# Kernel optimization log

Measured on AMD Instinct MI355X. Metric: run time of the kernel, lower is better.

Reference implementation:

```python
import jax, jax.numpy as jnp
import numpy as np
from jax import lax

B, R, C_FEAT, HF, WF = 4, 512, 256, 50, 50
NUM_CLASSES = 91
POOL = 7
SCALE = 1.0 / 16.0
IMG_H = IMG_W = 800.0
SCORE_THRESH = 0.05
NMS_THRESH = 0.5
DETS_PER_IMG = 100
TOPK_NMS = 2048  # fixed-size candidate set for static-shape NMS
BBOX_W = np.array([10.0, 10.0, 5.0, 5.0], np.float32)
BBOX_CLIP = float(np.log(1000.0 / 16.0))
MIN_SIZE = 0.01


def setup_inputs():
    key = jax.random.key(0)
    ks = jax.random.split(key, 8)
    features = jax.random.normal(ks[0], (B, C_FEAT, HF, WF), jnp.float32)
    cxy = jax.random.uniform(ks[1], (B, R, 2), jnp.float32, 50.0, 750.0)
    wh = jax.random.uniform(ks[2], (B, R, 2), jnp.float32, 20.0, 200.0)
    proposals = jnp.concatenate([cxy - wh / 2, cxy + wh / 2], axis=-1)
    d_in = C_FEAT * POOL * POOL
    def lin(k, fi, fo):
        return jax.random.normal(k, (fi, fo), jnp.float32) / np.sqrt(fi)
    return {
        'features': features, 'proposals': proposals,
        'W1': lin(ks[3], d_in, 1024), 'b1': jnp.zeros((1024,), jnp.float32),
        'W2': lin(ks[4], 1024, 1024), 'b2': jnp.zeros((1024,), jnp.float32),
        'Wc': lin(ks[5], 1024, NUM_CLASSES), 'bc': jnp.zeros((NUM_CLASSES,), jnp.float32),
        'Wr': lin(ks[6], 1024, 4 * NUM_CLASSES), 'br': jnp.zeros((4 * NUM_CLASSES,), jnp.float32),
    }


def roi_align(features, proposals):
    # features [B,C,H,W], proposals [B,R,4] in image coords -> [B*R, C*POOL*POOL]
    featT = jnp.transpose(features, (0, 2, 3, 1))  # [B,H,W,C]
    boxes = proposals * SCALE
    x1, y1, x2, y2 = (boxes[..., i] for i in range(4))
    bh = (y2 - y1) / POOL
    bw = (x2 - x1) / POOL
    centers = jnp.arange(POOL, dtype=jnp.float32) + 0.5
    ys = y1[..., None] + centers * bh[..., None]  # [B,R,P]
    xs = x1[..., None] + centers * bw[..., None]  # [B,R,P]

    def bil(fT, ys_b, xs_b):  # per-image bilinear sampling
        yy = jnp.broadcast_to(ys_b[:, :, None], (R, POOL, POOL))
        xx = jnp.broadcast_to(xs_b[:, None, :], (R, POOL, POOL))
        y = jnp.clip(yy, 0.0, HF - 1.0)
        x = jnp.clip(xx, 0.0, WF - 1.0)
        y0 = jnp.floor(y); x0 = jnp.floor(x)
        y0i = y0.astype(jnp.int32); x0i = x0.astype(jnp.int32)
        y1i = jnp.minimum(y0i + 1, HF - 1); x1i = jnp.minimum(x0i + 1, WF - 1)
        ly = y - y0; lx = x - x0; hy = 1.0 - ly; hx = 1.0 - lx
        f00 = fT[y0i, x0i]; f01 = fT[y0i, x1i]
        f10 = fT[y1i, x0i]; f11 = fT[y1i, x1i]  # [R,P,P,C]
        out = ((hy * hx)[..., None] * f00 + (hy * lx)[..., None] * f01 +
               (ly * hx)[..., None] * f10 + (ly * lx)[..., None] * f11)
        return out  # [R,P,P,C]

    pooled = jax.vmap(bil)(featT, ys, xs)  # [B,R,P,P,C]
    pooled = jnp.transpose(pooled, (0, 1, 4, 2, 3))  # [B,R,C,P,P] (torch layout)
    return pooled.reshape(B * R, -1)


def decode_boxes(box_reg, props):
    # box_reg [N, 4*NC], props [N,4] -> [N,NC,4]
    w = props[:, 2] - props[:, 0]
    h = props[:, 3] - props[:, 1]
    cx = props[:, 0] + 0.5 * w
    cy = props[:, 1] + 0.5 * h
    d = box_reg.reshape(-1, NUM_CLASSES, 4) / jnp.asarray(BBOX_W)
    dx, dy = d[..., 0], d[..., 1]
    dw = jnp.minimum(d[..., 2], BBOX_CLIP)
    dh = jnp.minimum(d[..., 3], BBOX_CLIP)
    pcx = dx * w[:, None] + cx[:, None]
    pcy = dy * h[:, None] + cy[:, None]
    pw = jnp.exp(dw) * w[:, None]
    ph = jnp.exp(dh) * h[:, None]
    return jnp.stack([pcx - 0.5 * pw, pcy - 0.5 * ph,
                      pcx + 0.5 * pw, pcy + 0.5 * ph], axis=-1)


def box_iou(a, b):
    area_a = (a[:, 2] - a[:, 0]) * (a[:, 3] - a[:, 1])
    area_b = (b[:, 2] - b[:, 0]) * (b[:, 3] - b[:, 1])
    lt = jnp.maximum(a[:, None, :2], b[None, :, :2])
    rb = jnp.minimum(a[:, None, 2:], b[None, :, 2:])
    wh = jnp.clip(rb - lt, 0.0)
    inter = wh[..., 0] * wh[..., 1]
    return inter / (area_a[:, None] + area_b[None, :] - inter)


def post_image(boxes, scores):
    # boxes [R,NC,4], scores [R,NC] -> fixed-size top DETS_PER_IMG detections
    x1 = jnp.clip(boxes[..., 0], 0.0, IMG_W)
    y1 = jnp.clip(boxes[..., 1], 0.0, IMG_H)
    x2 = jnp.clip(boxes[..., 2], 0.0, IMG_W)
    y2 = jnp.clip(boxes[..., 3], 0.0, IMG_H)
    boxes = jnp.stack([x1, y1, x2, y2], axis=-1)
    # drop background class 0, flatten (roi, class) candidates
    boxes = boxes[:, 1:].reshape(-1, 4)            # [R*(NC-1),4]
    scores = scores[:, 1:].reshape(-1)
    labels = jnp.broadcast_to(jnp.arange(1, NUM_CLASSES, dtype=jnp.int32)[None, :],
                              (R, NUM_CLASSES - 1)).reshape(-1)
    wv = boxes[:, 2] - boxes[:, 0]
    hv = boxes[:, 3] - boxes[:, 1]
    valid = (scores > SCORE_THRESH) & (wv >= MIN_SIZE) & (hv >= MIN_SIZE)
    cand = jnp.where(valid, scores, -1.0)
    top_s, top_i = lax.top_k(cand, TOPK_NMS)       # sorted desc by score
    b_k = boxes[top_i]
    l_k = labels[top_i]
    v_k = valid[top_i]
    # batched (per-class) NMS via label offset
    off = l_k.astype(jnp.float32)[:, None] * (IMG_W + 1.0)
    iou = box_iou(b_k + off, b_k + off)            # [K,K]
    idx = jnp.arange(TOPK_NMS)

    def body(i, keep):
        sup = jnp.any((idx < i) & keep & (iou[:, i] > NMS_THRESH))
        return keep.at[i].set(keep[i] & ~sup)

    keep = lax.fori_loop(0, TOPK_NMS, body, v_k)
    fs = jnp.where(keep, top_s, -1.0)
    out_s, out_i = lax.top_k(fs, DETS_PER_IMG)
    ok = out_s > 0.0
    out_b = jnp.where(ok[:, None], b_k[out_i], 0.0)
    out_l = jnp.where(ok, l_k[out_i], 0)
    out_s = jnp.where(ok, out_s, 0.0)
    return out_b, out_s, out_l


def reference(features, proposals, W1, b1, W2, b2, Wc, bc, Wr, br):
    x = roi_align(features, proposals)               # [B*R, C*49]
    x = jax.nn.relu(x @ W1 + b1)
    x = jax.nn.relu(x @ W2 + b2)
    class_logits = x @ Wc + bc                        # [B*R, NC]
    box_regression = x @ Wr + br                      # [B*R, 4*NC]
    props_flat = proposals.reshape(-1, 4)
    pred_boxes = decode_boxes(box_regression, props_flat).reshape(B, R, NUM_CLASSES, 4)
    pred_scores = jax.nn.softmax(class_logits, axis=-1).reshape(B, R, NUM_CLASSES)
    boxes, scores, labels = jax.vmap(post_image)(pred_boxes, pred_scores)
    return boxes, scores, labels


if __name__ == '__main__':
    out = reference(**setup_inputs())
    print([o.shape for o in out])
```

## Files before the change

kernel.cpp:

```cpp
#include <hip/hip_runtime.h>
#include <stdint.h>

#define NBI 4
#define RRI 512
#define NROI 2048
#define DIN 12544
#define BBOX_CLIP_F 4.135166556742356f

typedef _Float16 half8 __attribute__((ext_vector_type(8)));
typedef float f32x16 __attribute__((ext_vector_type(16)));

#define O_AH      10240000ull
#define O_AL      61620224ull
#define O_WTH     113000448ull
#define O_WTL     138690560ull
#define OZ        164380672ull
#define WS_NEED   189546496ull

#define O_X2H     0ull
#define O_X2L     2097152ull
#define O_X1H     O_AH
#define O_X1L     (O_AH + 4194304ull)
#define O_PBOX    O_AL
#define O_KEYS    (O_AL + 2949120ull)
#define O_NMSBOX  (O_AL + 3473408ull)
#define O_OUTBOX  (O_AL + 3604480ull)
#define O_SCORE   (O_AL + 3735552ull)
#define O_LABEL   (O_AL + 3768320ull)
#define O_CNT     (O_AL + 3801088ull)
#define O_MASK    (O_AL + 3802112ull)
#define O_WHH     O_WTH
#define O_WHL     (O_WTH + 1048576ull)
#define O_BH      (O_WTH + 2097152ull)
#define O_PARTH   (O_WTH + 2101248ull)
#define O_HEADF   (O_WTH + 18878464ull)
#define O_W2TH    OZ
#define O_W2TL    (OZ + 2097152ull)
#define O_PFC2    (OZ + 4194304ull)

__global__ void k_zero_out(float* __restrict__ out) {
  int i = blockIdx.x * 256 + threadIdx.x;
  if (i < 2400) out[i] = 0.0f;
}

__global__ void k_zero2(unsigned* __restrict__ keys32, unsigned* __restrict__ cnt) {
  int i = blockIdx.x * 256 + threadIdx.x;
  if (i < 131072) keys32[i] = 0u;
  if (i < 64) cnt[i] = 0u;
}

__global__ __launch_bounds__(256) void k_transpose(const float* __restrict__ f,
                                                   float* __restrict__ ft) {
  __shared__ float s[32][33];
  int b = blockIdx.z;
  int hw0 = blockIdx.x << 5;
  int c0 = blockIdx.y << 5;
  int tx = threadIdx.x & 31, ty = threadIdx.x >> 5;
#pragma unroll
  for (int j = 0; j < 32; j += 8) {
    int hw = hw0 + tx;
    if (hw < 2500) s[ty + j][tx] = f[((size_t)b * 256 + c0 + ty + j) * 2500 + hw];
  }
  __syncthreads();
#pragma unroll
  for (int j = 0; j < 32; j += 8) {
    int hw = hw0 + ty + j;
    if (hw < 2500) ft[((size_t)b * 2500 + hw) * 256 + c0 + tx] = s[tx][ty + j];
  }
}

__global__ __launch_bounds__(256) void k_wsplit(const float* __restrict__ W,
                                                _Float16* __restrict__ Th,
                                                _Float16* __restrict__ Tl, int K, int N) {
  __shared__ float s[64][68];
  int k0 = blockIdx.x << 6, n0 = blockIdx.y << 6;
  int t = threadIdx.x;
  int r = t >> 2, c4 = (t & 3) << 4;
#pragma unroll
  for (int j = 0; j < 16; j += 4) {
    float4 v = *(const float4*)(W + (size_t)(k0 + r) * N + n0 + c4 + j);
    s[r][c4 + j] = v.x; s[r][c4 + j + 1] = v.y; s[r][c4 + j + 2] = v.z; s[r][c4 + j + 3] = v.w;
  }
  __syncthreads();
  int nr = t >> 2, kc = (t & 3) << 4;
  half8 h8[2], l8[2];
#pragma unroll
  for (int j = 0; j < 16; ++j) {
    float v = s[kc + j][nr];
    _Float16 h = (_Float16)v;
    _Float16 lo = (_Float16)((v - (float)h) * 2048.0f);
    h8[j >> 3][j & 7] = h;
    l8[j >> 3][j & 7] = lo;
  }
  size_t base = (size_t)(n0 + nr) * K + k0 + kc;
  *(half8*)(Th + base) = h8[0]; *(half8*)(Th + base + 8) = h8[1];
  *(half8*)(Tl + base) = l8[0]; *(half8*)(Tl + base + 8) = l8[1];
}

__global__ __launch_bounds__(256) void k_wsplit_heads(const float* __restrict__ Wc,
                                                      const float* __restrict__ Wr,
                                                      const float* __restrict__ bcv,
                                                      const float* __restrict__ brv,
                                                      _Float16* __restrict__ Th,
                                                      _Float16* __restrict__ Tl,
                                                      float* __restrict__ bh) {
  int n = blockIdx.x;
  int t = threadIdx.x;
  for (int k = t; k < 1024; k += 256) {
    float v = (n < 91) ? Wc[(size_t)k * 91 + n]
                       : ((n < 455) ? Wr[(size_t)k * 364 + (n - 91)] : 0.0f);
    _Float16 h = (_Float16)v;
    Th[(size_t)n * 1024 + k] = h;
    Tl[(size_t)n * 1024 + k] = (_Float16)((v - (float)h) * 2048.0f);
  }
  if (t == 0) bh[n] = (n < 91) ? bcv[n] : ((n < 455) ? brv[n - 91] : 0.0f);
}

__global__ __launch_bounds__(256) void k_roialign(const float* __restrict__ ft,
                                                  const float* __restrict__ props,
                                                  _Float16* __restrict__ Ahg,
                                                  _Float16* __restrict__ Alg) {
  __shared__ float pool[DIN];
  __shared__ float lyA[7], lxA[7];
  __shared__ int y0A[7], y1A[7], x0A[7], x1A[7];
  int roi = blockIdx.x;
  int b = roi >> 9;
  const float* p = props + (size_t)roi * 4;
  float x1s = p[0] * 0.0625f, y1s = p[1] * 0.0625f;
  float x2s = p[2] * 0.0625f, y2s = p[3] * 0.0625f;
  float bh = (y2s - y1s) / 7.0f;
  float bw = (x2s - x1s) / 7.0f;
  int t = threadIdx.x;
  if (t < 7) {
    float y = y1s + ((float)t + 0.5f) * bh;
    y = fminf(fmaxf(y, 0.0f), 49.0f);
    float y0 = floorf(y);
    int y0i = (int)y0;
    y0A[t] = y0i; y1A[t] = min(y0i + 1, 49); lyA[t] = y - y0;
  } else if (t < 14) {
    int px = t - 7;
    float x = x1s + ((float)px + 0.5f) * bw;
    x = fminf(fmaxf(x, 0.0f), 49.0f);
    float x0 = floorf(x);
    int x0i = (int)x0;
    x0A[px] = x0i; x1A[px] = min(x0i + 1, 49); lxA[px] = x - x0;
  }
  __syncthreads();
  const float* fb = ft + (size_t)b * 2500 * 256;
  int c = t;
  for (int p49 = 0; p49 < 49; ++p49) {
    int py = p49 / 7, px = p49 - py * 7;
    int y0 = y0A[py], y1 = y1A[py], x0 = x0A[px], x1 = x1A[px];
    float ly = lyA[py], lx = lxA[px], hy = 1.0f - ly, hx = 1.0f - lx;
    float f00 = fb[(y0 * 50 + x0) * 256 + c];
    float f01 = fb[(y0 * 50 + x1) * 256 + c];
    float f10 = fb[(y1 * 50 + x0) * 256 + c];
    float f11 = fb[(y1 * 50 + x1) * 256 + c];
    pool[c * 49 + p49] = (hy * hx) * f00 + (hy * lx) * f01 + (ly * hx) * f10 + (ly * lx) * f11;
  }
  __syncthreads();
  _Float16* dh = Ahg + (size_t)roi * DIN;
  _Float16* dl = Alg + (size_t)roi * DIN;
  for (int i = t; i < DIN; i += 256) {
    float v = pool[i];
    _Float16 h = (_Float16)v;
    dh[i] = h;
    dl[i] = (_Float16)((v - (float)h) * 2048.0f);
  }
}

__global__ __launch_bounds__(256, 2) void k_mfma(const _Float16* __restrict__ Ah,
                                                 const _Float16* __restrict__ Al,
                                                 const _Float16* __restrict__ Bh,
                                                 const _Float16* __restrict__ Bl,
                                                 float* __restrict__ P0,
                                                 float* __restrict__ P2,
                                                 int K, int K2, int ldc, int MN) {
  __shared__ __align__(16) half8 sA[2][2][512];
  __shared__ __align__(16) half8 sB[2][2][512];
  int gx = gridDim.x, gy = gridDim.y;
  int nwg = gx * gy * gridDim.z;
  int lin = blockIdx.x + gx * (blockIdx.y + gy * blockIdx.z);
  int cpx = nwg >> 3;
  int nl = (lin & 7) * cpx + (lin >> 3);
  int sx = __ffs(gx) - 1, sy = __ffs(gy) - 1;
  int lx = nl & (gx - 1);
  int rest = nl >> sx;
  int ly = rest & (gy - 1);
  int lz = rest >> sy;
  int m0 = ly << 7, n0 = lx << 7;
  int kb = lz * K2;
  int t = threadIdx.x;
  int w = t >> 6, l = t & 63;
  int wr = w >> 1, wc = w & 1;
  int fr = l & 31, cgrp = l >> 5;
  int sr = t >> 1, sh = t & 1;
  const _Float16* gAh = Ah + (size_t)(m0 + sr) * K + kb + sh * 16;
  const _Float16* gAl = Al + (size_t)(m0 + sr) * K + kb + sh * 16;
  const _Float16* gBh = Bh + (size_t)(n0 + sr) * K + kb + sh * 16;
  const _Float16* gBl = Bl + (size_t)(n0 + sr) * K + kb + sh * 16;
  int ws0 = ((sr >> 5) * 4 + 2 * sh) * 32 + (sr & 31);
  int ws1 = ws0 + 32;
  int sa0 = wr * 256 + cgrp * 32 + fr;
  int sb0 = wc * 256 + cgrp * 32 + fr;
  f32x16 accH[2][2], accL[2][2];
#pragma unroll
  for (int i = 0; i < 2; ++i)
#pragma unroll
    for (int j = 0; j < 2; ++j)
#pragma unroll
      for (int r = 0; r < 16; ++r) { accH[i][j][r] = 0.0f; accL[i][j][r] = 0.0f; }
  half8 rAh0 = *(const half8*)gAh, rAh1 = *(const half8*)(gAh + 8);
  half8 rAl0 = *(const half8*)gAl, rAl1 = *(const half8*)(gAl + 8);
  half8 rBh0 = *(const half8*)gBh, rBh1 = *(const half8*)(gBh + 8);
  half8 rBl0 = *(const half8*)gBl, rBl1 = *(const half8*)(gBl + 8);
  sA[0][0][ws0] = rAh0; sA[0][0][ws1] = rAh1;
  sA[0][1][ws0] = rAl0; sA[0][1][ws1] = rAl1;
  sB[0][0][ws0] = rBh0; sB[0][0][ws1] = rBh1;
  sB[0][1][ws0] = rBl0; sB[0][1][ws1] = rBl1;
  if (32 < K2) {
    rAh0 = *(const half8*)(gAh + 32); rAh1 = *(const half8*)(gAh + 40);
    rAl0 = *(const half8*)(gAl + 32); rAl1 = *(const half8*)(gAl + 40);
    rBh0 = *(const half8*)(gBh + 32); rBh1 = *(const half8*)(gBh + 40);
    rBl0 = *(const half8*)(gBl + 32); rBl1 = *(const half8*)(gBl + 40);
  }
  __syncthreads();
  for (int kt = 0; kt < K2; kt += 32) {
    int buf = (kt >> 5) & 1;
    bool more = (kt + 32) < K2;
    if (more) {
      sA[buf ^ 1][0][ws0] = rAh0; sA[buf ^ 1][0][ws1] = rAh1;
      sA[buf ^ 1][1][ws0] = rAl0; sA[buf ^ 1][1][ws1] = rAl1;
      sB[buf ^ 1][0][ws0] = rBh0; sB[buf ^ 1][0][ws1] = rBh1;
      sB[buf ^ 1][1][ws0] = rBl0; sB[buf ^ 1][1][ws1] = rBl1;
    }
    if ((kt + 64) < K2) {
      rAh0 = *(const half8*)(gAh + kt + 64); rAh1 = *(const half8*)(gAh + kt + 72);
      rAl0 = *(const half8*)(gAl + kt + 64); rAl1 = *(const half8*)(gAl + kt + 72);
      rBh0 = *(const half8*)(gBh + kt + 64); rBh1 = *(const half8*)(gBh + kt + 72);
      rBl0 = *(const half8*)(gBl + kt + 64); rBl1 = *(const half8*)(gBl + kt + 72);
    }
#pragma unroll
    for (int s = 0; s < 2; ++s) {
      half8 aH[2], aL[2], bH[2], bL[2];
#pragma unroll
      for (int mf = 0; mf < 2; ++mf) {
        int sa = sa0 + mf * 128 + s * 64;
        aH[mf] = sA[buf][0][sa];
        aL[mf] = sA[buf][1][sa];
      }
#pragma unroll
      for (int nf = 0; nf < 2; ++nf) {
        int sb = sb0 + nf * 128 + s * 64;
        bH[nf] = sB[buf][0][sb];
        bL[nf] = sB[buf][1][sb];
      }
#pragma unroll
      for (int mf = 0; mf < 2; ++mf)
#pragma unroll
        for (int nf = 0; nf < 2; ++nf) {
          accH[mf][nf] =
              __builtin_amdgcn_mfma_f32_32x32x16_f16(aH[mf], bH[nf], accH[mf][nf], 0, 0, 0);
          accL[mf][nf] =
              __builtin_amdgcn_mfma_f32_32x32x16_f16(aH[mf], bL[nf], accL[mf][nf], 0, 0, 0);
          accL[mf][nf] =
              __builtin_amdgcn_mfma_f32_32x32x16_f16(aL[mf], bH[nf], accL[mf][nf], 0, 0, 0);
        }
    }
    if (more) __syncthreads();
  }
  float* Pz = (lz == 2) ? P2 : (P0 + (size_t)(lz == 3 ? 2 : lz) * MN);
  const float sc = 4.8828125e-4f;
#pragma unroll
  for (int mf = 0; mf < 2; ++mf)
#pragma unroll
    for (int nf = 0; nf < 2; ++nf) {
      int col = n0 + wc * 64 + nf * 32 + fr;
      int rbase = m0 + wr * 64 + mf * 32 + 4 * cgrp;
#pragma unroll
      for (int r = 0; r < 16; ++r) {
        int row = rbase + (r & 3) + ((r >> 2) << 3);
        Pz[(size_t)row * ldc + col] = accH[mf][nf][r] + accL[mf][nf][r] * sc;
      }
    }
}

__global__ void k_reduce_split(const float* __restrict__ P0, const float* __restrict__ P2,
                               const float* __restrict__ bias, _Float16* __restrict__ xh,
                               _Float16* __restrict__ xl, int S) {
  const int MN = 2048 * 1024;
  int i8 = blockIdx.x * 256 + threadIdx.x;
  size_t base = (size_t)i8 * 8;
  float v[8];
  {
    float4 a0 = *(const float4*)(P0 + base);
    float4 a1 = *(const float4*)(P0 + base + 4);
    float4 b0 = *(const float4*)(P0 + MN + base);
    float4 b1 = *(const float4*)(P0 + MN + base + 4);
    v[0] = a0.x + b0.x; v[1] = a0.y + b0.y; v[2] = a0.z + b0.z; v[3] = a0.w + b0.w;
    v[4] = a1.x + b1.x; v[5] = a1.y + b1.y; v[6] = a1.z + b1.z; v[7] = a1.w + b1.w;
  }
  if (S == 4) {
    float4 c0 = *(const float4*)(P2 + base);
    float4 c1 = *(const float4*)(P2 + base + 4);
    float4 d0 = *(const float4*)(P0 + 2 * (size_t)MN + base);
    float4 d1 = *(const float4*)(P0 + 2 * (size_t)MN + base + 4);
    v[0] = (v[0] + c0.x) + d0.x; v[1] = (v[1] + c0.y) + d0.y;
    v[2] = (v[2] + c0.z) + d0.z; v[3] = (v[3] + c0.w) + d0.w;
    v[4] = (v[4] + c1.x) + d1.x; v[5] = (v[5] + c1.y) + d1.y;
    v[6] = (v[6] + c1.z) + d1.z; v[7] = (v[7] + c1.w) + d1.w;
  }
  int cb = (int)(base & 1023);
  float4 b0 = *(const float4*)(bias + cb);
  float4 b1v = *(const float4*)(bias + cb + 4);
  v[0] += b0.x; v[1] += b0.y; v[2] += b0.z; v[3] += b0.w;
  v[4] += b1v.x; v[5] += b1v.y; v[6] += b1v.z; v[7] += b1v.w;
  half8 h8, l8;
#pragma unroll
  for (int j = 0; j < 8; ++j) {
    float x = fmaxf(v[j], 0.0f);
    _Float16 h = (_Float16)x;
    h8[j] = h;
    l8[j] = (_Float16)((x - (float)h) * 2048.0f);
  }
  *(half8*)(xh + base) = h8;
  *(half8*)(xl + base) = l8;
}

__global__ void k_headreduce(const float4* __restrict__ PH, const float* __restrict__ bh,
                             float4* __restrict__ head) {
  const int MN4 = 2048 * 512 / 4;
  int i = blockIdx.x * 256 + threadIdx.x;
  float4 p0 = PH[i], p1 = PH[i + MN4], p2 = PH[i + 3 * MN4], p3 = PH[i + 2 * MN4];
  const float4 b = *(const float4*)(bh + ((i & 127) << 2));
  float4 o;
  o.x = ((p0.x + p1.x) + p2.x) + p3.x + b.x;
  o.y = ((p0.y + p1.y) + p2.y) + p3.y + b.y;
  o.z = ((p0.z + p1.z) + p2.z) + p3.z + b.z;
  o.w = ((p0.w + p1.w) + p2.w) + p3.w + b.w;
  head[i] = o;
}

__global__ __launch_bounds__(256) void k_softmax_decode(const float* __restrict__ head,
                                                        const float* __restrict__ props,
                                                        float* __restrict__ pbox,
                                                        unsigned long long* __restrict__ keys,
                                                        unsigned* __restrict__ cnt) {
  int wave = threadIdx.x >> 6, lane = threadIdx.x & 63;
  int roi = (blockIdx.x << 2) + wave;
  const float* hr = head + (size_t)roi * 512;
  float l0 = hr[lane];
  float l1 = (lane < 27) ? hr[lane + 64] : -3.4e38f;
  float m = fmaxf(l0, l1);
#pragma unroll
  for (int off = 32; off; off >>= 1) m = fmaxf(m, __shfl_xor(m, off));
  float e0 = expf(l0 - m);
  float e1 = (lane < 27) ? expf(l1 - m) : 0.0f;
  float ssum = e0 + e1;
#pragma unroll
  for (int off = 32; off; off >>= 1) ssum += __shfl_xor(ssum, off);
  const float* pr = props + (size_t)roi * 4;
  float w = pr[2] - pr[0], h = pr[3] - pr[1];
  float cx = pr[0] + 0.5f * w, cy = pr[1] + 0.5f * h;
  int img = roi >> 9, rl = roi & 511;
#pragma unroll
  for (int half = 0; half < 2; ++half) {
    int c = lane + half * 64;
    float e = half ? e1 : e0;
    if (c >= 1 && c <= 90) {
      float score = e / ssum;
      const float* rg = hr + 91 + (c << 2);
      float dx = rg[0] / 10.0f, dy = rg[1] / 10.0f;
      float dw = fminf(rg[2] / 5.0f, BBOX_CLIP_F);
      float dh = fminf(rg[3] / 5.0f, BBOX_CLIP_F);
      float pcx = dx * w + cx, pcy = dy * h + cy;
      float pw = expf(dw) * w, ph = expf(dh) * h;
      float bx1 = pcx - 0.5f * pw, by1 = pcy - 0.5f * ph;
      float bx2 = pcx + 0.5f * pw, by2 = pcy + 0.5f * ph;
      bx1 = fminf(fmaxf(bx1, 0.0f), 800.0f);
      by1 = fminf(fmaxf(by1, 0.0f), 800.0f);
      bx2 = fminf(fmaxf(bx2, 0.0f), 800.0f);
      by2 = fminf(fmaxf(by2, 0.0f), 800.0f);
      float* pb = pbox + ((size_t)roi * 90 + (c - 1)) * 4;
      pb[0] = bx1; pb[1] = by1; pb[2] = bx2; pb[3] = by2;
      if (score > 0.05f && (bx2 - bx1) >= 0.01f && (by2 - by1) >= 0.01f) {
        unsigned pos = atomicAdd(cnt + img, 1u);
        unsigned idx = (unsigned)rl * 90u + (unsigned)(c - 1);
        unsigned su = __float_as_uint(score);
        su ^= (su >> 31) ? 0xFFFFFFFFu : 0x80000000u;
        keys[((size_t)img << 14) + pos] =
            ((unsigned long long)su << 32) | (unsigned long long)(0xFFFFFFFFu - idx);
      }
    }
  }
}

__global__ void k_sort(unsigned long long* __restrict__ keys, const unsigned* __restrict__ cnt) {
  extern __shared__ unsigned long long s[];
  int img = blockIdx.x, tid = threadIdx.x;
  unsigned long long* kb = keys + ((size_t)img << 14);
  unsigned n = cnt[img];
  unsigned np = 2048; while (np < n && np < 16384) np <<= 1;
  if (np <= 8192) {
    for (unsigned i = tid; i < np; i += 1024) s[i] = kb[i];
    __syncthreads();
    for (unsigned k = 2; k <= np; k <<= 1) {
      for (unsigned j = k >> 1; j; j >>= 1) {
        for (unsigned x = tid; x < (np >> 1); x += 1024) {
          unsigned i = ((x & ~(j - 1)) << 1) | (x & (j - 1));
          unsigned l = i | j;
          bool up = ((i & k) == 0);
          unsigned long long a = s[i], b = s[l];
          if ((a > b) == up) { s[i] = b; s[l] = a; }
        }
        __syncthreads();
      }
    }
    for (unsigned i = tid; i < np; i += 1024) kb[i] = s[i];
  } else {
    for (int ch = 0; ch < 2; ++ch) {
      unsigned base = (unsigned)ch << 13;
      for (unsigned i = tid; i < 8192; i += 1024) s[i] = kb[base + i];
      __syncthreads();
      for (unsigned k = 2; k <= 8192; k <<= 1) {
        for (unsigned j = k >> 1; j; j >>= 1) {
          for (unsigned x = tid; x < 4096; x += 1024) {
            unsigned i = ((x & ~(j - 1)) << 1) | (x & (j - 1));
            unsigned l = i | j;
            bool up = (((base + i) & k) == 0);
            unsigned long long a = s[i], b = s[l];
            if ((a > b) == up) { s[i] = b; s[l] = a; }
          }
          __syncthreads();
        }
      }
      for (unsigned i = tid; i < 8192; i += 1024) kb[base + i] = s[i];
      __syncthreads();
    }
    for (unsigned x = tid; x < 8192; x += 1024) {
      unsigned long long a = kb[x], b = kb[x + 8192];
      if (a > b) { kb[x] = b; kb[x + 8192] = a; }
    }
    __syncthreads();
    for (int ch = 0; ch < 2; ++ch) {
      unsigned base = (unsigned)ch << 13;
      for (unsigned i = tid; i < 8192; i += 1024) s[i] = kb[base + i];
      __syncthreads();
      for (unsigned j = 4096; j; j >>= 1) {
        for (unsigned x = tid; x < 4096; x += 1024) {
          unsigned i = ((x & ~(j - 1)) << 1) | (x & (j - 1));
          unsigned l = i | j;
          unsigned long long a = s[i], b = s[l];
          if (a > b) { s[i] = b; s[l] = a; }
        }
        __syncthreads();
      }
      for (unsigned i = tid; i < 8192; i += 1024) kb[base + i] = s[i];
      __syncthreads();
    }
  }
}

__global__ void k_gather(const unsigned long long* __restrict__ keys,
                         const unsigned* __restrict__ cnt, const float* __restrict__ pbox,
                         float4* __restrict__ nmsbox, float4* __restrict__ outbox,
                         float* __restrict__ score, float* __restrict__ label) {
  int g = blockIdx.x * 256 + threadIdx.x;
  int img = g >> 11, slot = g & 2047;
  unsigned n = cnt[img];
  unsigned neff = n > 2048u ? 2048u : n;
  unsigned np = 2048; while (np < n && np < 16384) np <<= 1;
  float4 bo = make_float4(0, 0, 0, 0), bx = make_float4(0, 0, 0, 0);
  float sc = -1.0f, lb = 0.0f;
  if ((unsigned)slot < neff) {
    unsigned long long key = keys[((size_t)img << 14) + (np - 1 - slot)];
    unsigned su = (unsigned)(key >> 32);
    su = (su & 0x80000000u) ? (su ^ 0x80000000u) : ~su;
    sc = __uint_as_float(su);
    unsigned idx = 0xFFFFFFFFu - (unsigned)(key & 0xFFFFFFFFull);
    unsigned rl = idx / 90u, c = idx - rl * 90u;
    const float* pb = pbox + ((size_t)((img << 9) + rl) * 90 + c) * 4;
    bx = *(const float4*)pb;
    float off = (float)(c + 1) * 801.0f;
    bo = make_float4(bx.x + off, bx.y + off, bx.z + off, bx.w + off);
    lb = (float)(c + 1);
  }
  nmsbox[g] = bo; outbox[g] = bx; score[g] = sc; label[g] = lb;
}

__global__ __launch_bounds__(256) void k_mask(const float* __restrict__ nmsbox,
                                              unsigned* __restrict__ mask) {
  __shared__ float bx[2048 * 4];
  int img = blockIdx.x >> 9;
  int i0 = (blockIdx.x & 511) << 2;
  const float4* src = (const float4*)(nmsbox + (size_t)img * 2048 * 4);
  for (int q = threadIdx.x; q < 2048; q += 256) ((float4*)bx)[q] = src[q];
  __syncthreads();
  int w = threadIdx.x & 63, ir = threadIdx.x >> 6;
  int i = i0 + ir;
  float ax1 = bx[i * 4], ay1 = bx[i * 4 + 1], ax2 = bx[i * 4 + 2], ay2 = bx[i * 4 + 3];
  float areaA = (ax2 - ax1) * (ay2 - ay1);
  unsigned bits = 0;
  for (int jj = 0; jj < 32; ++jj) {
    int j2 = (jj + w) & 31;
    int j = (w << 5) + j2;
    float b1 = bx[j * 4], b2 = bx[j * 4 + 1], b3 = bx[j * 4 + 2], b4 = bx[j * 4 + 3];
    float areaB = (b3 - b1) * (b4 - b2);
    float lx = fmaxf(ax1, b1), lyv = fmaxf(ay1, b2);
    float rx = fminf(ax2, b3), ry = fminf(ay2, b4);
    float iw = fmaxf(rx - lx, 0.0f), ih = fmaxf(ry - lyv, 0.0f);
    float inter = iw * ih;
    float iou = inter / (areaA + areaB - inter);
    if (iou > 0.5f) bits |= (1u << j2);
  }
  mask[((size_t)img * 2048 + i) * 64 + w] = bits;
}

__global__ void k_scan(const unsigned* __restrict__ mask, const unsigned* __restrict__ cnt,
                       const float* __restrict__ outbox, const float* __restrict__ score,
                       const float* __restrict__ label, float* __restrict__ dout) {
  int img = blockIdx.x, lane = threadIdx.x;
  unsigned n = cnt[img];
  unsigned neff = n > 2048u ? 2048u : n;
  unsigned base = (unsigned)lane * 32u;
  unsigned rem;
  if (base + 32u <= neff) rem = 0u;
  else if (base >= neff) rem = 0xFFFFFFFFu;
  else rem = ~((1u << (neff - base)) - 1u);
  const unsigned* mrow = mask + (size_t)img * 2048 * 64;
  unsigned row = (neff > 0) ? mrow[lane] : 0u;
  int outc = 0;
  for (int i = 0; i < (int)neff; ++i) {
    unsigned nextrow = (i + 1 < (int)neff) ? mrow[(size_t)(i + 1) * 64 + lane] : 0u;
    unsigned wrd = __shfl(rem, i >> 5);
    bool kept = ((wrd >> (i & 31)) & 1u) == 0u;
    if (kept) {
      rem |= row;
      if (lane < 4)
        dout[(size_t)(img * 100 + outc) * 4 + lane] = outbox[((size_t)img * 2048 + i) * 4 + lane];
      if (lane == 0) {
        dout[1600 + img * 100 + outc] = score[img * 2048 + i];
        dout[2000 + img * 100 + outc] = label[img * 2048 + i];
      }
      ++outc;
      if (outc >= 100) break;
    }
    row = nextrow;
  }
}

extern "C" void kernel_launch(void* const* d_in, const int* in_sizes, int n_in,
                              void* d_out, int out_size, void* d_ws, size_t ws_size,
                              hipStream_t stream) {
  if (ws_size < WS_NEED) return;

  const float* features  = (const float*)d_in[0];
  const float* proposals = (const float*)d_in[1];
  const float* W1 = (const float*)d_in[2];
  const float* b1 = (const float*)d_in[3];
  const float* W2 = (const float*)d_in[4];
  const float* b2 = (const float*)d_in[5];
  const float* Wc = (const float*)d_in[6];
  const float* bc = (const float*)d_in[7];
  const float* Wr = (const float*)d_in[8];
  const float* br = (const float*)d_in[9];
  float* out = (float*)d_out;
  char* ws = (char*)d_ws;

  float* featT = (float*)(ws + 0);
  _Float16* Ahg = (_Float16*)(ws + O_AH);
  _Float16* Alg = (_Float16*)(ws + O_AL);
  _Float16* Wth = (_Float16*)(ws + O_WTH);
  _Float16* Wtl = (_Float16*)(ws + O_WTL);
  float* partZ = (float*)(ws + OZ);
  float* partF = (float*)(ws + 0);
  _Float16* x1h = (_Float16*)(ws + O_X1H);
  _Float16* x1l = (_Float16*)(ws + O_X1L);
  _Float16* W2th = (_Float16*)(ws + O_W2TH);
  _Float16* W2tl = (_Float16*)(ws + O_W2TL);
  float* partC = (float*)(ws + O_PFC2);
  _Float16* x2h = (_Float16*)(ws + O_X2H);
  _Float16* x2l = (_Float16*)(ws + O_X2L);
  _Float16* whh = (_Float16*)(ws + O_WHH);
  _Float16* whl = (_Float16*)(ws + O_WHL);
  float* bhv   = (float*)(ws + O_BH);
  float* partH = (float*)(ws + O_PARTH);
  float* partH2 = (float*)(ws + O_PARTH + 3ull * 4194304ull);
  float* head  = (float*)(ws + O_HEADF);
  float* pbox  = (float*)(ws + O_PBOX);
  unsigned long long* keys = (unsigned long long*)(ws + O_KEYS);
  float* nmsbox = (float*)(ws + O_NMSBOX);
  float* outbox = (float*)(ws + O_OUTBOX);
  float* scorea = (float*)(ws + O_SCORE);
  float* labela = (float*)(ws + O_LABEL);
  unsigned* cnt = (unsigned*)(ws + O_CNT);
  unsigned* maska = (unsigned*)(ws + O_MASK);

  k_zero_out<<<10, 256, 0, stream>>>(out);
  k_transpose<<<dim3(79, 8, 4), 256, 0, stream>>>(features, featT);
  k_wsplit<<<dim3(196, 16), 256, 0, stream>>>(W1, Wth, Wtl, 12544, 1024);
  k_roialign<<<2048, 256, 0, stream>>>(featT, proposals, Ahg, Alg);
  k_mfma<<<dim3(8, 16, 4), 256, 0, stream>>>(Ahg, Alg, Wth, Wtl, partZ, partF,
                                             12544, 3136, 1024, 2048 * 1024);
  k_reduce_split<<<1024, 256, 0, stream>>>(partZ, partF, b1, x1h, x1l, 4);
  k_wsplit<<<dim3(16, 16), 256, 0, stream>>>(W2, W2th, W2tl, 1024, 1024);
  k_wsplit_heads<<<512, 256, 0, stream>>>(Wc, Wr, bc, br, whh, whl, bhv);
  k_mfma<<<dim3(8, 16, 2), 256, 0, stream>>>(x1h, x1l, W2th, W2tl, partC, partC,
                                             1024, 512, 1024, 2048 * 1024);
  k_reduce_split<<<1024, 256, 0, stream>>>(partC, partC, b2, x2h, x2l, 2);
  k_mfma<<<dim3(4, 16, 4), 256, 0, stream>>>(x2h, x2l, whh, whl, partH, partH2,
                                             1024, 256, 512, 2048 * 512);
  k_headreduce<<<1024, 256, 0, stream>>>((const float4*)partH, bhv, (float4*)head);
  k_zero2<<<512, 256, 0, stream>>>((unsigned*)keys, cnt);
  k_softmax_decode<<<512, 256, 0, stream>>>(head, proposals, pbox, keys, cnt);
  k_sort<<<4, 1024, 65536, stream>>>(keys, cnt);
  k_gather<<<32, 256, 0, stream>>>(keys, cnt, pbox, (float4*)nmsbox, (float4*)outbox,
                                   scorea, labela);
  k_mask<<<2048, 256, 0, stream>>>(nmsbox, maska);
  k_scan<<<4, 64, 0, stream>>>(maska, cnt, outbox, scorea, labela, out);
}
```

Baseline: 383.8 us.

## Use direct global-to-LDS loads in MFMA GEMM and fuse small prep kernels

The MFMA GEMM now stages A and B tiles with `global_load_lds` straight into shared memory, replacing the register round-trip and its separate LDS stores. Several tiny launches are folded into neighbours: output zeroing moves into the transpose, W2 split plus head-weight split plus key zeroing become one kernel, and the head partial reduction is done inside softmax/decode. The RoI-align output conversion writes 8-wide half vectors instead of scalars. These aim to cut launch overhead, an extra global round-trip for the head logits, and GEMM load latency. The catch is that direct-to-LDS loads depend on correct wait and barrier ordering, and softmax now re-reads four partials per element.

```diff
diff --git a/kernel.cpp b/kernel.cpp
--- a/kernel.cpp
+++ b/kernel.cpp
@@ -9,6 +9,10 @@
 
 typedef _Float16 half8 __attribute__((ext_vector_type(8)));
 typedef float f32x16 __attribute__((ext_vector_type(16)));
+
+#define GLDS(g, l)                                                                   \
+  __builtin_amdgcn_global_load_lds((const __attribute__((address_space(1))) void*)(g), \
+                                   (__attribute__((address_space(3))) void*)(l), 16, 0, 0)
 
 #define O_AH      10240000ull
 #define O_AL      61620224ull
@@ -33,28 +37,21 @@
 #define O_WHL     (O_WTH + 1048576ull)
 #define O_BH      (O_WTH + 2097152ull)
 #define O_PARTH   (O_WTH + 2101248ull)
-#define O_HEADF   (O_WTH + 18878464ull)
 #define O_W2TH    OZ
 #define O_W2TL    (OZ + 2097152ull)
 #define O_PFC2    (OZ + 4194304ull)
 
-__global__ void k_zero_out(float* __restrict__ out) {
-  int i = blockIdx.x * 256 + threadIdx.x;
-  if (i < 2400) out[i] = 0.0f;
-}
-
-__global__ void k_zero2(unsigned* __restrict__ keys32, unsigned* __restrict__ cnt) {
-  int i = blockIdx.x * 256 + threadIdx.x;
-  if (i < 131072) keys32[i] = 0u;
-  if (i < 64) cnt[i] = 0u;
-}
-
 __global__ __launch_bounds__(256) void k_transpose(const float* __restrict__ f,
-                                                   float* __restrict__ ft) {
+                                                   float* __restrict__ ft,
+                                                   float* __restrict__ out) {
   __shared__ float s[32][33];
   int b = blockIdx.z;
   int hw0 = blockIdx.x << 5;
   int c0 = blockIdx.y << 5;
+  if (blockIdx.y == 0 && blockIdx.z == 0 && blockIdx.x < 10) {
+    int i = blockIdx.x * 256 + threadIdx.x;
+    if (i < 2400) out[i] = 0.0f;
+  }
   int tx = threadIdx.x & 31, ty = threadIdx.x >> 5;
 #pragma unroll
   for (int j = 0; j < 32; j += 8) {
@@ -97,23 +94,56 @@
   *(half8*)(Tl + base) = l8[0]; *(half8*)(Tl + base + 8) = l8[1];
 }
 
-__global__ __launch_bounds__(256) void k_wsplit_heads(const float* __restrict__ Wc,
-                                                      const float* __restrict__ Wr,
-                                                      const float* __restrict__ bcv,
-                                                      const float* __restrict__ brv,
-                                                      _Float16* __restrict__ Th,
-                                                      _Float16* __restrict__ Tl,
-                                                      float* __restrict__ bh) {
-  int n = blockIdx.x;
+__global__ __launch_bounds__(256) void k_prep2(const float* __restrict__ W2,
+                                               const float* __restrict__ Wc,
+                                               const float* __restrict__ Wr,
+                                               const float* __restrict__ bcv,
+                                               const float* __restrict__ brv,
+                                               _Float16* __restrict__ T2h,
+                                               _Float16* __restrict__ T2l,
+                                               _Float16* __restrict__ Th,
+                                               _Float16* __restrict__ Tl,
+                                               float* __restrict__ bh,
+                                               unsigned* __restrict__ keys32,
+                                               unsigned* __restrict__ cnt) {
+  int blk = blockIdx.x;
   int t = threadIdx.x;
-  for (int k = t; k < 1024; k += 256) {
-    float v = (n < 91) ? Wc[(size_t)k * 91 + n]
-                       : ((n < 455) ? Wr[(size_t)k * 364 + (n - 91)] : 0.0f);
-    _Float16 h = (_Float16)v;
-    Th[(size_t)n * 1024 + k] = h;
-    Tl[(size_t)n * 1024 + k] = (_Float16)((v - (float)h) * 2048.0f);
-  }
-  if (t == 0) bh[n] = (n < 91) ? bcv[n] : ((n < 455) ? brv[n - 91] : 0.0f);
+  if (blk < 256) {
+    __shared__ float s[64][68];
+    int k0 = (blk & 15) << 6, n0 = (blk >> 4) << 6;
+    int r = t >> 2, c4 = (t & 3) << 4;
+#pragma unroll
+    for (int j = 0; j < 16; j += 4) {
+      float4 v = *(const float4*)(W2 + (size_t)(k0 + r) * 1024 + n0 + c4 + j);
+      s[r][c4 + j] = v.x; s[r][c4 + j + 1] = v.y; s[r][c4 + j + 2] = v.z; s[r][c4 + j + 3] = v.w;
+    }
+    __syncthreads();
+    int nr = t >> 2, kc = (t & 3) << 4;
+    half8 h8[2], l8[2];
+#pragma unroll
+    for (int j = 0; j < 16; ++j) {
+      float v = s[kc + j][nr];
+      _Float16 h = (_Float16)v;
+      _Float16 lo = (_Float16)((v - (float)h) * 2048.0f);
+      h8[j >> 3][j & 7] = h;
+      l8[j >> 3][j & 7] = lo;
+    }
+    size_t base = (size_t)(n0 + nr) * 1024 + k0 + kc;
+    *(half8*)(T2h + base) = h8[0]; *(half8*)(T2h + base + 8) = h8[1];
+    *(half8*)(T2l + base) = l8[0]; *(half8*)(T2l + base + 8) = l8[1];
+  } else {
+    int n = blk - 256;
+    keys32[(n << 8) + t] = 0u;
+    if (n == 0 && t < 64) cnt[t] = 0u;
+    for (int k = t; k < 1024; k += 256) {
+      float v = (n < 91) ? Wc[(size_t)k * 91 + n]
+                         : ((n < 455) ? Wr[(size_t)k * 364 + (n - 91)] : 0.0f);
+      _Float16 h = (_Float16)v;
+      Th[(size_t)n * 1024 + k] = h;
+      Tl[(size_t)n * 1024 + k] = (_Float16)((v - (float)h) * 2048.0f);
+    }
+    if (t == 0) bh[n] = (n < 91) ? bcv[n] : ((n < 455) ? brv[n - 91] : 0.0f);
+  }
 }
 
 __global__ __launch_bounds__(256) void k_roialign(const float* __restrict__ ft,
@@ -161,11 +191,17 @@
   __syncthreads();
   _Float16* dh = Ahg + (size_t)roi * DIN;
   _Float16* dl = Alg + (size_t)roi * DIN;
-  for (int i = t; i < DIN; i += 256) {
-    float v = pool[i];
-    _Float16 h = (_Float16)v;
-    dh[i] = h;
-    dl[i] = (_Float16)((v - (float)h) * 2048.0f);
+  for (int i8 = t; i8 < 1568; i8 += 256) {
+    half8 h8v, l8v;
+#pragma unroll
+    for (int j = 0; j < 8; ++j) {
+      float v = pool[i8 * 8 + j];
+      _Float16 h = (_Float16)v;
+      h8v[j] = h;
+      l8v[j] = (_Float16)((v - (float)h) * 2048.0f);
+    }
+    *(half8*)(dh + (size_t)i8 * 8) = h8v;
+    *(half8*)(dl + (size_t)i8 * 8) = l8v;
   }
 }
 
@@ -194,13 +230,14 @@
   int w = t >> 6, l = t & 63;
   int wr = w >> 1, wc = w & 1;
   int fr = l & 31, cgrp = l >> 5;
-  int sr = t >> 1, sh = t & 1;
-  const _Float16* gAh = Ah + (size_t)(m0 + sr) * K + kb + sh * 16;
-  const _Float16* gAl = Al + (size_t)(m0 + sr) * K + kb + sh * 16;
-  const _Float16* gBh = Bh + (size_t)(n0 + sr) * K + kb + sh * 16;
-  const _Float16* gBl = Bl + (size_t)(n0 + sr) * K + kb + sh * 16;
-  int ws0 = ((sr >> 5) * 4 + 2 * sh) * 32 + (sr & 31);
-  int ws1 = ws0 + 32;
+  int rowA = m0 + 32 * w + (l & 31);
+  int rowB = n0 + 32 * w + (l & 31);
+  int kc0 = (l >> 5) << 3;
+  const _Float16* gAh = Ah + (size_t)rowA * K + kb + kc0;
+  const _Float16* gAl = Al + (size_t)rowA * K + kb + kc0;
+  const _Float16* gBh = Bh + (size_t)rowB * K + kb + kc0;
+  const _Float16* gBl = Bl + (size_t)rowB * K + kb + kc0;
+  int sh0 = 128 * w, sh1 = 128 * w + 64;
   int sa0 = wr * 256 + cgrp * 32 + fr;
   int sb0 = wc * 256 + cgrp * 32 + fr;
   f32x16 accH[2][2], accL[2][2];
@@ -210,35 +247,21 @@
     for (int j = 0; j < 2; ++j)
 #pragma unroll
       for (int r = 0; r < 16; ++r) { accH[i][j][r] = 0.0f; accL[i][j][r] = 0.0f; }
-  half8 rAh0 = *(const half8*)gAh, rAh1 = *(const half8*)(gAh + 8);
-  half8 rAl0 = *(const half8*)gAl, rAl1 = *(const half8*)(gAl + 8);
-  half8 rBh0 = *(const half8*)gBh, rBh1 = *(const half8*)(gBh + 8);
-  half8 rBl0 = *(const half8*)gBl, rBl1 = *(const half8*)(gBl + 8);
-  sA[0][0][ws0] = rAh0; sA[0][0][ws1] = rAh1;
-  sA[0][1][ws0] = rAl0; sA[0][1][ws1] = rAl1;
-  sB[0][0][ws0] = rBh0; sB[0][0][ws1] = rBh1;
-  sB[0][1][ws0] = rBl0; sB[0][1][ws1] = rBl1;
-  if (32 < K2) {
-    rAh0 = *(const half8*)(gAh + 32); rAh1 = *(const half8*)(gAh + 40);
-    rAl0 = *(const half8*)(gAl + 32); rAl1 = *(const half8*)(gAl + 40);
-    rBh0 = *(const half8*)(gBh + 32); rBh1 = *(const half8*)(gBh + 40);
-    rBl0 = *(const half8*)(gBl + 32); rBl1 = *(const half8*)(gBl + 40);
-  }
+  GLDS(gAh, &sA[0][0][sh0]); GLDS(gAh + 16, &sA[0][0][sh1]);
+  GLDS(gAl, &sA[0][1][sh0]); GLDS(gAl + 16, &sA[0][1][sh1]);
+  GLDS(gBh, &sB[0][0][sh0]); GLDS(gBh + 16, &sB[0][0][sh1]);
+  GLDS(gBl, &sB[0][1][sh0]); GLDS(gBl + 16, &sB[0][1][sh1]);
   __syncthreads();
   for (int kt = 0; kt < K2; kt += 32) {
     int buf = (kt >> 5) & 1;
+    int nb = buf ^ 1;
     bool more = (kt + 32) < K2;
     if (more) {
-      sA[buf ^ 1][0][ws0] = rAh0; sA[buf ^ 1][0][ws1] = rAh1;
-      sA[buf ^ 1][1][ws0] = rAl0; sA[buf ^ 1][1][ws1] = rAl1;
-      sB[buf ^ 1][0][ws0] = rBh0; sB[buf ^ 1][0][ws1] = rBh1;
-      sB[buf ^ 1][1][ws0] = rBl0; sB[buf ^ 1][1][ws1] = rBl1;
-    }
-    if ((kt + 64) < K2) {
-      rAh0 = *(const half8*)(gAh + kt + 64); rAh1 = *(const half8*)(gAh + kt + 72);
-      rAl0 = *(const half8*)(gAl + kt + 64); rAl1 = *(const half8*)(gAl + kt + 72);
-      rBh0 = *(const half8*)(gBh + kt + 64); rBh1 = *(const half8*)(gBh + kt + 72);
-      rBl0 = *(const half8*)(gBl + kt + 64); rBl1 = *(const half8*)(gBl + kt + 72);
+      int o = kt + 32;
+      GLDS(gAh + o, &sA[nb][0][sh0]); GLDS(gAh + o + 16, &sA[nb][0][sh1]);
+      GLDS(gAl + o, &sA[nb][1][sh0]); GLDS(gAl + o + 16, &sA[nb][1][sh1]);
+      GLDS(gBh + o, &sB[nb][0][sh0]); GLDS(gBh + o + 16, &sB[nb][0][sh1]);
+      GLDS(gBl + o, &sB[nb][1][sh0]); GLDS(gBl + o + 16, &sB[nb][1][sh1]);
     }
 #pragma unroll
     for (int s = 0; s < 2; ++s) {
@@ -327,30 +350,20 @@
   *(half8*)(xl + base) = l8;
 }
 
-__global__ void k_headreduce(const float4* __restrict__ PH, const float* __restrict__ bh,
-                             float4* __restrict__ head) {
-  const int MN4 = 2048 * 512 / 4;
-  int i = blockIdx.x * 256 + threadIdx.x;
-  float4 p0 = PH[i], p1 = PH[i + MN4], p2 = PH[i + 3 * MN4], p3 = PH[i + 2 * MN4];
-  const float4 b = *(const float4*)(bh + ((i & 127) << 2));
-  float4 o;
-  o.x = ((p0.x + p1.x) + p2.x) + p3.x + b.x;
-  o.y = ((p0.y + p1.y) + p2.y) + p3.y + b.y;
-  o.z = ((p0.z + p1.z) + p2.z) + p3.z + b.z;
-  o.w = ((p0.w + p1.w) + p2.w) + p3.w + b.w;
-  head[i] = o;
-}
-
-__global__ __launch_bounds__(256) void k_softmax_decode(const float* __restrict__ head,
+__global__ __launch_bounds__(256) void k_softmax_decode(const float* __restrict__ PH,
+                                                        const float* __restrict__ bh,
                                                         const float* __restrict__ props,
                                                         float* __restrict__ pbox,
                                                         unsigned long long* __restrict__ keys,
                                                         unsigned* __restrict__ cnt) {
+  const int MNh = 2048 * 512;
   int wave = threadIdx.x >> 6, lane = threadIdx.x & 63;
   int roi = (blockIdx.x << 2) + wave;
-  const float* hr = head + (size_t)roi * 512;
-  float l0 = hr[lane];
-  float l1 = (lane < 27) ? hr[lane + 64] : -3.4e38f;
+  size_t eb = (size_t)roi * 512;
+#define HREAD(e) ((((PH[(e)] + PH[(e) + MNh]) + PH[(e) + 3 * (size_t)MNh]) + \
+                   PH[(e) + 2 * (size_t)MNh]) + bh[(e) - eb])
+  float l0 = HREAD(eb + lane);
+  float l1 = (lane < 27) ? HREAD(eb + lane + 64) : -3.4e38f;
   float m = fmaxf(l0, l1);
 #pragma unroll
   for (int off = 32; off; off >>= 1) m = fmaxf(m, __shfl_xor(m, off));
@@ -369,10 +382,10 @@
     float e = half ? e1 : e0;
     if (c >= 1 && c <= 90) {
       float score = e / ssum;
-      const float* rg = hr + 91 + (c << 2);
-      float dx = rg[0] / 10.0f, dy = rg[1] / 10.0f;
-      float dw = fminf(rg[2] / 5.0f, BBOX_CLIP_F);
-      float dh = fminf(rg[3] / 5.0f, BBOX_CLIP_F);
+      size_t rg = eb + 91 + (c << 2);
+      float dx = HREAD(rg + 0) / 10.0f, dy = HREAD(rg + 1) / 10.0f;
+      float dw = fminf(HREAD(rg + 2) / 5.0f, BBOX_CLIP_F);
+      float dh = fminf(HREAD(rg + 3) / 5.0f, BBOX_CLIP_F);
       float pcx = dx * w + cx, pcy = dy * h + cy;
       float pw = expf(dw) * w, ph = expf(dh) * h;
       float bx1 = pcx - 0.5f * pw, by1 = pcy - 0.5f * ph;
@@ -393,6 +406,7 @@
       }
     }
   }
+#undef HREAD
 }
 
 __global__ void k_sort(unsigned long long* __restrict__ keys, const unsigned* __restrict__ cnt) {
@@ -586,7 +600,6 @@
   float* bhv   = (float*)(ws + O_BH);
   float* partH = (float*)(ws + O_PARTH);
   float* partH2 = (float*)(ws + O_PARTH + 3ull * 4194304ull);
-  float* head  = (float*)(ws + O_HEADF);
   float* pbox  = (float*)(ws + O_PBOX);
   unsigned long long* keys = (unsigned long long*)(ws + O_KEYS);
   float* nmsbox = (float*)(ws + O_NMSBOX);
@@ -596,23 +609,20 @@
   unsigned* cnt = (unsigned*)(ws + O_CNT);
   unsigned* maska = (unsigned*)(ws + O_MASK);
 
-  k_zero_out<<<10, 256, 0, stream>>>(out);
-  k_transpose<<<dim3(79, 8, 4), 256, 0, stream>>>(features, featT);
+  k_transpose<<<dim3(79, 8, 4), 256, 0, stream>>>(features, featT, out);
   k_wsplit<<<dim3(196, 16), 256, 0, stream>>>(W1, Wth, Wtl, 12544, 1024);
   k_roialign<<<2048, 256, 0, stream>>>(featT, proposals, Ahg, Alg);
   k_mfma<<<dim3(8, 16, 4), 256, 0, stream>>>(Ahg, Alg, Wth, Wtl, partZ, partF,
                                              12544, 3136, 1024, 2048 * 1024);
   k_reduce_split<<<1024, 256, 0, stream>>>(partZ, partF, b1, x1h, x1l, 4);
-  k_wsplit<<<dim3(16, 16), 256, 0, stream>>>(W2, W2th, W2tl, 1024, 1024);
-  k_wsplit_heads<<<512, 256, 0, stream>>>(Wc, Wr, bc, br, whh, whl, bhv);
+  k_prep2<<<768, 256, 0, stream>>>(W2, Wc, Wr, bc, br, W2th, W2tl, whh, whl, bhv,
+                                   (unsigned*)keys, cnt);
   k_mfma<<<dim3(8, 16, 2), 256, 0, stream>>>(x1h, x1l, W2th, W2tl, partC, partC,
                                              1024, 512, 1024, 2048 * 1024);
   k_reduce_split<<<1024, 256, 0, stream>>>(partC, partC, b2, x2h, x2l, 2);
   k_mfma<<<dim3(4, 16, 4), 256, 0, stream>>>(x2h, x2l, whh, whl, partH, partH2,
                                              1024, 256, 512, 2048 * 512);
-  k_headreduce<<<1024, 256, 0, stream>>>((const float4*)partH, bhv, (float4*)head);
-  k_zero2<<<512, 256, 0, stream>>>((unsigned*)keys, cnt);
-  k_softmax_decode<<<512, 256, 0, stream>>>(head, proposals, pbox, keys, cnt);
+  k_softmax_decode<<<512, 256, 0, stream>>>(partH, bhv, proposals, pbox, keys, cnt);
   k_sort<<<4, 1024, 65536, stream>>>(keys, cnt);
   k_gather<<<32, 256, 0, stream>>>(keys, cnt, pbox, (float4*)nmsbox, (float4*)outbox,
                                    scorea, labela);
```

New measurement: 395.2 us. 3.0% more time.
